# Optimization experiments

Hardware: AMD Instinct MI355X
Metric: run time of the kernel (lower is better)

The kernel has to match this reference:

```python
import jax, jax.numpy as jnp
import numpy as np

D = 64            # number of devices (leaves hold D/8 each)
B = 65536         # batch of states
FEAT = 5 + 4 * D  # 261
HID = 128


def setup_inputs() -> dict:
    key = jax.random.key(0)
    ks = jax.random.split(key, 10)
    def nrm(k, shape, s=0.1):
        return jax.random.normal(k, shape, jnp.float32) * s
    return {
        "x": jax.random.normal(ks[0], (B, FEAT), jnp.float32),
        # gate params per depth d: 2^d nodes, weight dim 5 + 4*D/2^d
        "w0": nrm(ks[1], (1, 5 + 4 * D)),
        "b0": jnp.zeros((1,), jnp.float32),
        "w1": nrm(ks[2], (2, 5 + 4 * (D // 2))),
        "b1": jnp.zeros((2,), jnp.float32),
        "w2": nrm(ks[3], (4, 5 + 4 * (D // 4))),
        "b2": jnp.zeros((4,), jnp.float32),
        # leaf prob_dist (torch inits to zeros; random here for a non-trivial baseline)
        "leaf_probs": nrm(ks[4], (8, D // 8), 1.0),
        # critic MLP
        "Wc1": nrm(ks[5], (FEAT, HID)),
        "bc1": jnp.zeros((HID,), jnp.float32),
        "Wc2": nrm(ks[6], (HID, 1)),
        "bc2": jnp.zeros((1,), jnp.float32),
    }


def reference(x, w0, b0, w1, b1, w2, b2, leaf_probs, Wc1, bc1, Wc2, bc2):
    # Batched deterministic ClusterTree routing (exploration disabled).
    x5 = x[:, :5]                       # (B, 5) global features
    dev = x[:, 5:].reshape(B, D, 4)     # (B, D, 4) per-device features
    node = jnp.zeros((B,), jnp.int32)   # current node index at each depth
    cum = jnp.ones((B,), x.dtype)       # product of gate values along path
    for d, (wd, bd) in enumerate([(w0, b0), (w1, b1), (w2, b2)]):
        nd = D >> d                     # devices per node at this depth
        off = node * nd                 # contiguous-cluster start offset
        idx = off[:, None] + jnp.arange(nd)                     # (B, nd)
        dslice = jnp.take_along_axis(dev, idx[:, :, None], 1)   # (B, nd, 4)
        w = wd[node]                    # (B, 5 + 4*nd)
        gate = (jnp.sum(x5 * w[:, :5], -1)
                + jnp.sum(dslice.reshape(B, -1) * w[:, 5:], -1)
                + bd[node])
        val = jax.nn.sigmoid(gate)
        cum = cum * val                 # torch: val * child_output, recursively
        node = node * 2 + (val >= 0.5).astype(jnp.int32)
    p = cum[:, None] * leaf_probs[node]                 # (B, D//8)
    v = jax.nn.relu(x @ Wc1 + bc1) @ Wc2 + bc2          # (B, 1) critic
    return p, v
```

## Files before the change

### kernel.cpp

```cpp
#include <hip/hip_runtime.h>
#include <hip/hip_bf16.h>
#include <stdint.h>

#define NB    65536
#define FEATN 261
#define HIDN  128
#define NSTEP 17
#define SROW  296

#define ROWSG 128
#define NTHRG 512

typedef __attribute__((ext_vector_type(8)))  short bf16x8;
typedef __attribute__((ext_vector_type(16))) float f32x16;
typedef float f32x4u __attribute__((ext_vector_type(4), aligned(4)));

#define MFMA32(A, B, C) __builtin_amdgcn_mfma_f32_32x32x16_bf16(A, B, C, 0, 0, 0)

__global__ void prep_B(const float* __restrict__ Wc1, uint16_t* __restrict__ wsB) {
    int t = blockIdx.x * blockDim.x + threadIdx.x;
    if (t >= NSTEP * 4 * 64) return;
    int p = t >> 6, l = t & 63;
    int s = p >> 2, nt = p & 3;
    int n = nt * 32 + (l & 31);
    int kb = 16 * s + 8 * (l >> 5);
    uint16_t hw[8];
    #pragma unroll
    for (int j = 0; j < 8; ++j) {
        int k = kb + j;
        float v = (k < FEATN) ? Wc1[(size_t)k * HIDN + n] : 0.f;
        __hip_bfloat16 b = __float2bfloat16(v);
        hw[j] = *reinterpret_cast<uint16_t*>(&b);
    }
    *reinterpret_cast<uint4*>(wsB + (size_t)p * 512 + l * 8) =
        *reinterpret_cast<uint4*>(hw);
}

__global__ void tree_kernel(
    const float* __restrict__ x,
    const float* __restrict__ w0, const float* __restrict__ b0,
    const float* __restrict__ w1, const float* __restrict__ b1,
    const float* __restrict__ w2, const float* __restrict__ b2,
    const float* __restrict__ leaf,
    float* __restrict__ out_p)
{
    const int tid = threadIdx.x;
    const int s   = tid & 15;
    const int row = blockIdx.x * 16 + (tid >> 4);
    const float* xr = x + (size_t)row * FEATN;

    f32x4u w0q[4];
    #pragma unroll
    for (int j = 0; j < 4; ++j)
        w0q[j] = *reinterpret_cast<const f32x4u*>(w0 + 4 * s + 64 * j);
    const float w0t = (s < 5) ? w0[256 + s] : 0.f;

    f32x4u w1aq[2], w1bq[2];
    #pragma unroll
    for (int j = 0; j < 2; ++j) {
        w1aq[j] = *reinterpret_cast<const f32x4u*>(w1 + 5 + 8 * s + 4 * j);
        w1bq[j] = *reinterpret_cast<const f32x4u*>(w1 + 133 + 5 + 8 * s + 4 * j);
    }
    const float w1a5 = (s < 5) ? w1[s]       : 0.f;
    const float w1b5 = (s < 5) ? w1[133 + s] : 0.f;

    f32x4u w2q0 = *reinterpret_cast<const f32x4u*>(w2 +  0 * 69 + 5 + 4 * s);
    f32x4u w2q1 = *reinterpret_cast<const f32x4u*>(w2 +  1 * 69 + 5 + 4 * s);
    f32x4u w2q2 = *reinterpret_cast<const f32x4u*>(w2 +  2 * 69 + 5 + 4 * s);
    f32x4u w2q3 = *reinterpret_cast<const f32x4u*>(w2 +  3 * 69 + 5 + 4 * s);
    float w25_0 = (s < 5) ? w2[0 * 69 + s] : 0.f;
    float w25_1 = (s < 5) ? w2[1 * 69 + s] : 0.f;
    float w25_2 = (s < 5) ? w2[2 * 69 + s] : 0.f;
    float w25_3 = (s < 5) ? w2[3 * 69 + s] : 0.f;

    f32x4u xq[4];
    #pragma unroll
    for (int j = 0; j < 4; ++j)
        xq[j] = *reinterpret_cast<const f32x4u*>(xr + 4 * s + 64 * j);
    const float xt  = (s < 5) ? xr[256 + s] : 0.f;
    const float xs5 = (s < 5) ? xr[s]       : 0.f;

    float part = xt * w0t;
    #pragma unroll
    for (int j = 0; j < 4; ++j)
        #pragma unroll
        for (int c = 0; c < 4; ++c)
            part += xq[j][c] * w0q[j][c];
    part += __shfl_xor(part, 1);
    part += __shfl_xor(part, 2);
    part += __shfl_xor(part, 4);
    part += __shfl_xor(part, 8);
    float gate = part + b0[0];
    int node = (gate >= 0.f) ? 1 : 0;
    float cum = 1.f / (1.f + __expf(-gate));

    {
        const float* base = xr + 5 + 128 * node + 8 * s;
        f32x4u xw0 = *reinterpret_cast<const f32x4u*>(base);
        f32x4u xw1 = *reinterpret_cast<const f32x4u*>(base + 4);
        part = xs5 * (node ? w1b5 : w1a5);
        #pragma unroll
        for (int c = 0; c < 4; ++c) {
            part += xw0[c] * (node ? w1bq[0][c] : w1aq[0][c]);
            part += xw1[c] * (node ? w1bq[1][c] : w1aq[1][c]);
        }
        part += __shfl_xor(part, 1);
        part += __shfl_xor(part, 2);
        part += __shfl_xor(part, 4);
        part += __shfl_xor(part, 8);
        gate = part + b1[node];
        cum *= 1.f / (1.f + __expf(-gate));
        node = node * 2 + ((gate >= 0.f) ? 1 : 0);
    }
    {
        f32x4u xv2 = *reinterpret_cast<const f32x4u*>(xr + 5 + 64 * node + 4 * s);
        f32x4u t0 = (node & 1) ? w2q1 : w2q0;
        f32x4u t1 = (node & 1) ? w2q3 : w2q2;
        f32x4u wsel = (node & 2) ? t1 : t0;
        float w5a = (node & 1) ? w25_1 : w25_0;
        float w5b = (node & 1) ? w25_3 : w25_2;
        float w5sel = (node & 2) ? w5b : w5a;
        part = xs5 * w5sel;
        #pragma unroll
        for (int c = 0; c < 4; ++c) part += xv2[c] * wsel[c];
        part += __shfl_xor(part, 1);
        part += __shfl_xor(part, 2);
        part += __shfl_xor(part, 4);
        part += __shfl_xor(part, 8);
        gate = part + b2[node];
        cum *= 1.f / (1.f + __expf(-gate));
        node = node * 2 + ((gate >= 0.f) ? 1 : 0);
    }
    if (s < 8)
        out_p[(size_t)row * 8 + s] = cum * leaf[node * 8 + s];
}

__global__ __launch_bounds__(NTHRG, 4) void critic_gemm(
    const float* __restrict__ x,
    const uint16_t* __restrict__ wsB,
    const float* __restrict__ bc1, const float* __restrict__ Wc2,
    const float* __restrict__ bc2,
    float* __restrict__ out_v)
{
    __shared__ uint16_t Axs[ROWSG * SROW];
    __shared__ float bc1s[HIDN];
    __shared__ float wc2s[HIDN];
    __shared__ float vpart[ROWSG * 2];

    const int tid = threadIdx.x;
    const int rowBase = blockIdx.x * ROWSG;

    if (tid < HIDN) { bc1s[tid] = bc1[tid]; wc2s[tid] = Wc2[tid]; }
    if (tid < ROWSG) {
        uint16_t* rp = Axs + tid * SROW;
        rp[261] = 0;
        *reinterpret_cast<uint32_t*>(rp + 262) = 0u;
        uint4 z; z.x = z.y = z.z = z.w = 0u;
        *reinterpret_cast<uint4*>(rp + 264) = z;
        *reinterpret_cast<uint4*>(rp + 272) = z;
        *reinterpret_cast<uint4*>(rp + 280) = z;
        *reinterpret_cast<uint4*>(rp + 288) = z;
    }

    {
        const float4* xg4 = reinterpret_cast<const float4*>(x + (size_t)rowBase * FEATN);
        for (int i = tid; i < ROWSG * FEATN / 4; i += NTHRG) {
            float4 v = xg4[i];
            const float* vv = reinterpret_cast<const float*>(&v);
            int f = i << 2;
            int m = f / FEATN;
            int k = f - m * FEATN;
            if (k + 3 < FEATN) {
                uint16_t* dst = Axs + m * SROW + k;
                #pragma unroll
                for (int j = 0; j < 4; ++j) {
                    __hip_bfloat16 b = __float2bfloat16(vv[j]);
                    dst[j] = *reinterpret_cast<uint16_t*>(&b);
                }
            } else {
                #pragma unroll
                for (int j = 0; j < 4; ++j) {
                    if (k >= FEATN) { k -= FEATN; m++; }
                    __hip_bfloat16 b = __float2bfloat16(vv[j]);
                    Axs[m * SROW + k] = *reinterpret_cast<uint16_t*>(&b);
                    k++;
                }
            }
        }
    }
    __syncthreads();

    const int lane = tid & 63;
    const int w    = tid >> 6;
    const int mt   = w >> 1;
    const int nh   = w & 1;

    f32x16 acc0 = {}, acc1 = {};
    const uint16_t* arow = Axs + (mt * 32 + (lane & 31)) * SROW + (lane >> 5) * 8;
    const uint16_t* bgl  = wsB + (size_t)(2 * nh) * 512 + lane * 8;

    bf16x8 ca[2], cb0[2], cb1[2], na[2], nb0[2], nb1[2];
    #pragma unroll
    for (int d = 0; d < 2; ++d) {
        ca[d]  = *reinterpret_cast<const bf16x8*>(arow + d * 16);
        cb0[d] = *reinterpret_cast<const bf16x8*>(bgl + (size_t)(d * 4)     * 512);
        cb1[d] = *reinterpret_cast<const bf16x8*>(bgl + (size_t)(d * 4 + 1) * 512);
    }
    #pragma unroll
    for (int g = 0; g < 8; ++g) {
        if (g < 7) {
            #pragma unroll
            for (int d = 0; d < 2; ++d) {
                const int st = 2 * g + 2 + d;
                na[d]  = *reinterpret_cast<const bf16x8*>(arow + st * 16);
                nb0[d] = *reinterpret_cast<const bf16x8*>(bgl + (size_t)(st * 4)     * 512);
                nb1[d] = *reinterpret_cast<const bf16x8*>(bgl + (size_t)(st * 4 + 1) * 512);
            }
        } else {
            na[0]  = *reinterpret_cast<const bf16x8*>(arow + 16 * 16);
            nb0[0] = *reinterpret_cast<const bf16x8*>(bgl + (size_t)(16 * 4)     * 512);
            nb1[0] = *reinterpret_cast<const bf16x8*>(bgl + (size_t)(16 * 4 + 1) * 512);
        }
        #pragma unroll
        for (int d = 0; d < 2; ++d) {
            acc0 = MFMA32(ca[d], cb0[d], acc0);
            acc1 = MFMA32(ca[d], cb1[d], acc1);
        }
        #pragma unroll
        for (int d = 0; d < 2; ++d) { ca[d] = na[d]; cb0[d] = nb0[d]; cb1[d] = nb1[d]; }
    }
    acc0 = MFMA32(ca[0], cb0[0], acc0);
    acc1 = MFMA32(ca[0], cb1[0], acc1);

    {
        const int c = lane & 31;
        const int q = lane >> 5;
        const int n0 = 2 * nh * 32 + c;
        const int n1 = n0 + 32;
        const float bb0 = bc1s[n0], ww0 = wc2s[n0];
        const float bb1 = bc1s[n1], ww1 = wc2s[n1];

        float pv[16];
        #pragma unroll
        for (int reg = 0; reg < 16; ++reg) {
            float h0 = acc0[reg] + bb0; h0 = h0 > 0.f ? h0 : 0.f;
            float h1 = acc1[reg] + bb1; h1 = h1 > 0.f ? h1 : 0.f;
            float t = h0 * ww0 + h1 * ww1;
            t += __shfl_xor(t, 1);
            t += __shfl_xor(t, 2);
            t += __shfl_xor(t, 4);
            t += __shfl_xor(t, 8);
            t += __shfl_xor(t, 16);
            pv[reg] = t;
        }
        #pragma unroll
        for (int reg = 0; reg < 16; ++reg) {
            if (c == reg) {
                int row_local = (reg & 3) + 8 * (reg >> 2) + 4 * q;
                vpart[(mt * 32 + row_local) * 2 + nh] = pv[reg];
            }
        }
    }
    __syncthreads();
    if (tid < ROWSG)
        out_v[rowBase + tid] = vpart[tid * 2] + vpart[tid * 2 + 1] + bc2[0];
}

extern "C" void kernel_launch(void* const* d_in, const int* in_sizes, int n_in,
                              void* d_out, int out_size, void* d_ws, size_t ws_size,
                              hipStream_t stream) {
    const float* x    = (const float*)d_in[0];
    const float* w0   = (const float*)d_in[1];
    const float* b0   = (const float*)d_in[2];
    const float* w1   = (const float*)d_in[3];
    const float* b1   = (const float*)d_in[4];
    const float* w2   = (const float*)d_in[5];
    const float* b2   = (const float*)d_in[6];
    const float* leaf = (const float*)d_in[7];
    const float* Wc1  = (const float*)d_in[8];
    const float* bc1  = (const float*)d_in[9];
    const float* Wc2  = (const float*)d_in[10];
    const float* bc2  = (const float*)d_in[11];

    uint16_t* wsB = (uint16_t*)d_ws;

    float* out_p = (float*)d_out;
    float* out_v = out_p + (size_t)NB * 8;

    prep_B<<<(NSTEP * 4 * 64 + 255) / 256, 256, 0, stream>>>(Wc1, wsB);
    tree_kernel<<<NB / 16, 256, 0, stream>>>(
        x, w0, b0, w1, b1, w2, b2, leaf, out_p);
    critic_gemm<<<NB / ROWSG, NTHRG, 0, stream>>>(
        x, wsB, bc1, Wc2, bc2, out_v);
}
```

Before: 141.5 us.

## Fold weight prep into tree kernel, restructure critic staging and MFMA loads

```diff
diff --git a/kernel.cpp b/kernel.cpp
--- a/kernel.cpp
+++ b/kernel.cpp
@@ -17,23 +17,9 @@
 
 #define MFMA32(A, B, C) __builtin_amdgcn_mfma_f32_32x32x16_bf16(A, B, C, 0, 0, 0)
 
-__global__ void prep_B(const float* __restrict__ Wc1, uint16_t* __restrict__ wsB) {
-    int t = blockIdx.x * blockDim.x + threadIdx.x;
-    if (t >= NSTEP * 4 * 64) return;
-    int p = t >> 6, l = t & 63;
-    int s = p >> 2, nt = p & 3;
-    int n = nt * 32 + (l & 31);
-    int kb = 16 * s + 8 * (l >> 5);
-    uint16_t hw[8];
-    #pragma unroll
-    for (int j = 0; j < 8; ++j) {
-        int k = kb + j;
-        float v = (k < FEATN) ? Wc1[(size_t)k * HIDN + n] : 0.f;
-        __hip_bfloat16 b = __float2bfloat16(v);
-        hw[j] = *reinterpret_cast<uint16_t*>(&b);
-    }
-    *reinterpret_cast<uint4*>(wsB + (size_t)p * 512 + l * 8) =
-        *reinterpret_cast<uint4*>(hw);
+__device__ __forceinline__ uint16_t f2b(float v) {
+    __hip_bfloat16 b = __float2bfloat16(v);
+    return *reinterpret_cast<uint16_t*>(&b);
 }
 
 __global__ void tree_kernel(
@@ -42,9 +28,30 @@
     const float* __restrict__ w1, const float* __restrict__ b1,
     const float* __restrict__ w2, const float* __restrict__ b2,
     const float* __restrict__ leaf,
+    const float* __restrict__ Wc1, uint16_t* __restrict__ wsB,
     float* __restrict__ out_p)
 {
     const int tid = threadIdx.x;
+
+    if (blockIdx.x < 17) {
+        int t = blockIdx.x * 256 + tid;
+        if (t < NSTEP * 4 * 64) {
+            int p = t >> 6, l = t & 63;
+            int s = p >> 2, nt = p & 3;
+            int n = nt * 32 + (l & 31);
+            int kb = 16 * s + 8 * (l >> 5);
+            uint16_t hw[8];
+            #pragma unroll
+            for (int j = 0; j < 8; ++j) {
+                int k = kb + j;
+                float v = (k < FEATN) ? Wc1[(size_t)k * HIDN + n] : 0.f;
+                hw[j] = f2b(v);
+            }
+            *reinterpret_cast<uint4*>(wsB + (size_t)p * 512 + l * 8) =
+                *reinterpret_cast<uint4*>(hw);
+        }
+    }
+
     const int s   = tid & 15;
     const int row = blockIdx.x * 16 + (tid >> 4);
     const float* xr = x + (size_t)row * FEATN;
@@ -135,7 +142,7 @@
         out_p[(size_t)row * 8 + s] = cum * leaf[node * 8 + s];
 }
 
-__global__ __launch_bounds__(NTHRG, 4) void critic_gemm(
+__global__ __launch_bounds__(NTHRG, 2) void critic_gemm(
     const float* __restrict__ x,
     const uint16_t* __restrict__ wsB,
     const float* __restrict__ bc1, const float* __restrict__ Wc2,
@@ -163,28 +170,19 @@
     }
 
     {
-        const float4* xg4 = reinterpret_cast<const float4*>(x + (size_t)rowBase * FEATN);
-        for (int i = tid; i < ROWSG * FEATN / 4; i += NTHRG) {
-            float4 v = xg4[i];
-            const float* vv = reinterpret_cast<const float*>(&v);
-            int f = i << 2;
-            int m = f / FEATN;
-            int k = f - m * FEATN;
-            if (k + 3 < FEATN) {
-                uint16_t* dst = Axs + m * SROW + k;
-                #pragma unroll
-                for (int j = 0; j < 4; ++j) {
-                    __hip_bfloat16 b = __float2bfloat16(vv[j]);
-                    dst[j] = *reinterpret_cast<uint16_t*>(&b);
-                }
+        for (int idx = tid; idx < ROWSG * 66; idx += NTHRG) {
+            int row = idx / 66;
+            int seg = idx - row * 66;
+            const float* src = x + (size_t)(rowBase + row) * FEATN + 4 * seg;
+            uint16_t* dst = Axs + row * SROW + 4 * seg;
+            if (seg < 65) {
+                f32x4u v = *reinterpret_cast<const f32x4u*>(src);
+                uint32_t p0 = (uint32_t)f2b(v[0]) | ((uint32_t)f2b(v[1]) << 16);
+                uint32_t p1 = (uint32_t)f2b(v[2]) | ((uint32_t)f2b(v[3]) << 16);
+                uint2 pk; pk.x = p0; pk.y = p1;
+                *reinterpret_cast<uint2*>(dst) = pk;
             } else {
-                #pragma unroll
-                for (int j = 0; j < 4; ++j) {
-                    if (k >= FEATN) { k -= FEATN; m++; }
-                    __hip_bfloat16 b = __float2bfloat16(vv[j]);
-                    Axs[m * SROW + k] = *reinterpret_cast<uint16_t*>(&b);
-                    k++;
-                }
+                dst[0] = f2b(src[0]);
             }
         }
     }
@@ -195,42 +193,23 @@
     const int mt   = w >> 1;
     const int nh   = w & 1;
 
-    f32x16 acc0 = {}, acc1 = {};
     const uint16_t* arow = Axs + (mt * 32 + (lane & 31)) * SROW + (lane >> 5) * 8;
     const uint16_t* bgl  = wsB + (size_t)(2 * nh) * 512 + lane * 8;
 
-    bf16x8 ca[2], cb0[2], cb1[2], na[2], nb0[2], nb1[2];
-    #pragma unroll
-    for (int d = 0; d < 2; ++d) {
-        ca[d]  = *reinterpret_cast<const bf16x8*>(arow + d * 16);
-        cb0[d] = *reinterpret_cast<const bf16x8*>(bgl + (size_t)(d * 4)     * 512);
-        cb1[d] = *reinterpret_cast<const bf16x8*>(bgl + (size_t)(d * 4 + 1) * 512);
-    }
-    #pragma unroll
-    for (int g = 0; g < 8; ++g) {
-        if (g < 7) {
-            #pragma unroll
-            for (int d = 0; d < 2; ++d) {
-                const int st = 2 * g + 2 + d;
-                na[d]  = *reinterpret_cast<const bf16x8*>(arow + st * 16);
-                nb0[d] = *reinterpret_cast<const bf16x8*>(bgl + (size_t)(st * 4)     * 512);
-                nb1[d] = *reinterpret_cast<const bf16x8*>(bgl + (size_t)(st * 4 + 1) * 512);
-            }
-        } else {
-            na[0]  = *reinterpret_cast<const bf16x8*>(arow + 16 * 16);
-            nb0[0] = *reinterpret_cast<const bf16x8*>(bgl + (size_t)(16 * 4)     * 512);
-            nb1[0] = *reinterpret_cast<const bf16x8*>(bgl + (size_t)(16 * 4 + 1) * 512);
-        }
-        #pragma unroll
-        for (int d = 0; d < 2; ++d) {
-            acc0 = MFMA32(ca[d], cb0[d], acc0);
-            acc1 = MFMA32(ca[d], cb1[d], acc1);
-        }
-        #pragma unroll
-        for (int d = 0; d < 2; ++d) { ca[d] = na[d]; cb0[d] = nb0[d]; cb1[d] = nb1[d]; }
-    }
-    acc0 = MFMA32(ca[0], cb0[0], acc0);
-    acc1 = MFMA32(ca[0], cb1[0], acc1);
+    bf16x8 af[NSTEP], bf0[NSTEP], bf1[NSTEP];
+    #pragma unroll
+    for (int s = 0; s < NSTEP; ++s) {
+        af[s]  = *reinterpret_cast<const bf16x8*>(arow + s * 16);
+        bf0[s] = *reinterpret_cast<const bf16x8*>(bgl + (size_t)(s * 4)     * 512);
+        bf1[s] = *reinterpret_cast<const bf16x8*>(bgl + (size_t)(s * 4 + 1) * 512);
+    }
+
+    f32x16 acc0 = {}, acc1 = {};
+    #pragma unroll
+    for (int s = 0; s < NSTEP; ++s) {
+        acc0 = MFMA32(af[s], bf0[s], acc0);
+        acc1 = MFMA32(af[s], bf1[s], acc1);
+    }
 
     {
         const int c = lane & 31;
@@ -287,9 +266,8 @@
     float* out_p = (float*)d_out;
     float* out_v = out_p + (size_t)NB * 8;
 
-    prep_B<<<(NSTEP * 4 * 64 + 255) / 256, 256, 0, stream>>>(Wc1, wsB);
     tree_kernel<<<NB / 16, 256, 0, stream>>>(
-        x, w0, b0, w1, b1, w2, b2, leaf, out_p);
+        x, w0, b0, w1, b1, w2, b2, leaf, Wc1, wsB, out_p);
     critic_gemm<<<NB / ROWSG, NTHRG, 0, stream>>>(
         x, wsB, bc1, Wc2, bc2, out_v);
 }
```

New measurement: 137.7 us. -2.7%, faster.
